# Kernel optimization log

Measured on AMD Instinct MI355X. Metric: run time of the kernel, lower is better.

Reference implementation:

```python
import jax, jax.numpy as jnp
import numpy as np

NH, KD, VD, C = 8, 64, 64, 256

def conv1x1(x, w, b):
    # x: (B,C,D,H,W), w: (O,C), b: (O,)
    return jnp.einsum('bcdhw,oc->bodhw', x, w) + b[None, :, None, None, None]

def setup_inputs() -> dict:
    key = jax.random.key(0)
    ks = jax.random.split(key, 8)
    B, D, H, W = 2, 32, 32, 32
    s = 0.02
    return {
        'x': jax.random.normal(ks[0], (B, C, D, H, W), jnp.float32),
        'q_w': jax.random.normal(ks[1], (NH * KD, C), jnp.float32) * s,
        'q_b': jnp.zeros((NH * KD,), jnp.float32),
        'kv_w': jax.random.normal(ks[2], (KD + VD, C), jnp.float32) * s,
        'kv_b': jnp.zeros((KD + VD,), jnp.float32),
        'proj_w': jax.random.normal(ks[3], (C, NH * VD), jnp.float32) * s,
        'proj_b': jnp.zeros((C,), jnp.float32),
        'layer_scale': jnp.full((C, 1, 1, 1), 1e-5, jnp.float32),
    }

def reference(x, q_w, q_b, kv_w, kv_b, proj_w, proj_b, layer_scale):
    B, Cc, D, H, W = x.shape
    scale = VD ** -0.5
    # q: (B, nh, D, H, W, kd) -> flatten(3,5) -> (B, nh, D, H*W*kd)
    q = conv1x1(x, q_w, q_b).reshape(B, NH, KD, D, H, W).transpose(0, 1, 3, 4, 5, 2)
    q = q.reshape(B, NH, D, H * W * KD)
    kv = conv1x1(x, kv_w, kv_b)  # (B, kd+vd, D, H, W)
    k = kv[:, :KD].transpose(0, 2, 3, 4, 1).reshape(B, D, H * W * KD)  # shared across heads
    v = kv[:, KD:].transpose(0, 2, 3, 4, 1).reshape(B, D, H * W * VD)
    attn = jax.nn.softmax(jnp.einsum('bnqf,bkf->bnqk', q, k) * scale, axis=-1)  # (B,nh,D,D)
    o = jnp.einsum('bnqk,bkf->bnqf', attn, v)  # (B, nh, D, H*W*vd)
    # transpose(1,2) then row-major reshape, exactly as torch
    o = o.transpose(0, 2, 1, 3).reshape(B, D, H, W, NH * VD).transpose(0, 4, 1, 2, 3)
    out = conv1x1(o, proj_w, proj_b)
    return out * layer_scale[None]
```

## Files before the change

kernel.cpp:

```cpp
#include <hip/hip_runtime.h>
#include <math.h>

#define SS 32768
#define FQL_LDS_BYTES 147456

typedef _Float16 half4v __attribute__((ext_vector_type(4)));
typedef _Float16 half8v __attribute__((ext_vector_type(8)));
typedef float float4v __attribute__((ext_vector_type(4)));

__device__ __forceinline__ void gload16(const void* g, void* l) {
    __builtin_amdgcn_global_load_lds(
        (const __attribute__((address_space(1))) unsigned int*)g,
        (__attribute__((address_space(3))) unsigned int*)l, 16, 0, 0);
}

__global__ __launch_bounds__(256)
void cvt_x_kernel(const float* __restrict__ x, _Float16* __restrict__ x_t)
{
    __shared__ float ls[64][65];
    const int b = blockIdx.z, c0 = blockIdx.y * 64, s0 = blockIdx.x * 64;
    const int t = threadIdx.x;
    const int tr = t >> 4, tc = t & 15;
#pragma unroll
    for (int p = 0; p < 4; p++) {
        int c_l = p * 16 + tr;
        float4v v = *(const float4v*)(x + (size_t)(b * 256 + c0 + c_l) * SS + s0 + tc * 4);
        ls[c_l][tc * 4 + 0] = v.x;
        ls[c_l][tc * 4 + 1] = v.y;
        ls[c_l][tc * 4 + 2] = v.z;
        ls[c_l][tc * 4 + 3] = v.w;
    }
    __syncthreads();
#pragma unroll
    for (int p = 0; p < 4; p++) {
        int s_l = p * 16 + tr;
        half4v h;
        h.x = (_Float16)ls[tc * 4 + 0][s_l];
        h.y = (_Float16)ls[tc * 4 + 1][s_l];
        h.z = (_Float16)ls[tc * 4 + 2][s_l];
        h.w = (_Float16)ls[tc * 4 + 3][s_l];
        *(half4v*)(x_t + ((size_t)b * SS + s0 + s_l) * 256 + c0 + tc * 4) = h;
    }
}

__global__ __launch_bounds__(256)
void cvt_w3_kernel(const float* __restrict__ s0, _Float16* __restrict__ d0,
                   const float* __restrict__ s1, _Float16* __restrict__ d1,
                   const float* __restrict__ s2, _Float16* __restrict__ d2)
{
    int bx = blockIdx.x;
    const float* s; _Float16* d; int base;
    if (bx < 128)      { s = s0; d = d0; base = bx; }
    else if (bx < 160) { s = s1; d = d1; base = bx - 128; }
    else               { s = s2; d = d2; base = bx - 160; }
    int i = (base * 256 + threadIdx.x) * 4;
    float4v v = *(const float4v*)(s + i);
    half4v h;
    h.x = (_Float16)v.x; h.y = (_Float16)v.y; h.z = (_Float16)v.z; h.w = (_Float16)v.w;
    *(half4v*)(d + i) = h;
}

__global__ __launch_bounds__(256)
void convkv_kernel(const _Float16* __restrict__ x_t,
                   const _Float16* __restrict__ wkv,
                   const float* __restrict__ kv_b,
                   _Float16* __restrict__ kv_t)
{
    __shared__ _Float16 smem[128 * 136];
    _Float16* const Ws = smem;
    _Float16* const Xs = smem + 128 * 64;
    const int b = blockIdx.y;
    const int s0 = blockIdx.x * 128;
    const int t = threadIdx.x;
    const int w = t >> 6, l = t & 63;
    const int om = (w & 1) * 64, sn = (w >> 1) * 64;

    const int lr = l >> 3;
    const int gch = ((l & 7) - lr) & 7;
    const int m15 = l & 15;
    const int sl0 = ((((l >> 4) + (l & 7)) & 7)) * 8;
    const int sl1 = ((((l >> 4) + 4 + (l & 7)) & 7)) * 8;

    float4v acc[4][4];
#pragma unroll
    for (int i = 0; i < 4; i++)
#pragma unroll
        for (int j = 0; j < 4; j++) acc[i][j] = (float4v){0.f, 0.f, 0.f, 0.f};

    const _Float16* wg = wkv + (size_t)(32 * w + lr) * 256 + gch * 8;
    const _Float16* xg = x_t + ((size_t)b * SS + s0 + 32 * w + lr) * 256 + gch * 8;
    _Float16* wl = &Ws[(32 * w) * 64];
    _Float16* xl = &Xs[(32 * w) * 64];

    for (int c0 = 0; c0 < 256; c0 += 64) {
#pragma unroll
        for (int rb = 0; rb < 4; rb++) {
            gload16(wg + (size_t)rb * 8 * 256 + c0, wl + rb * 8 * 64);
            gload16(xg + (size_t)rb * 8 * 256 + c0, xl + rb * 8 * 64);
        }
        __syncthreads();
#pragma unroll
        for (int ks = 0; ks < 2; ks++) {
            const int sl = ks ? sl1 : sl0;
            half8v a[4], bb[4];
#pragma unroll
            for (int i = 0; i < 4; i++)
                a[i] = *(const half8v*)&Ws[(om + i * 16 + m15) * 64 + sl];
#pragma unroll
            for (int j = 0; j < 4; j++)
                bb[j] = *(const half8v*)&Xs[(sn + j * 16 + m15) * 64 + sl];
#pragma unroll
            for (int i = 0; i < 4; i++)
#pragma unroll
                for (int j = 0; j < 4; j++)
                    acc[i][j] = __builtin_amdgcn_mfma_f32_16x16x32_f16(a[i], bb[j], acc[i][j], 0, 0, 0);
        }
        __syncthreads();
    }
    const int qd = l >> 4, m = l & 15;
#pragma unroll
    for (int i = 0; i < 4; i++) {
        float bv[4];
#pragma unroll
        for (int r = 0; r < 4; r++) bv[r] = kv_b[om + i * 16 + qd * 4 + r];
#pragma unroll
        for (int j = 0; j < 4; j++) {
            half4v h;
            h.x = (_Float16)(acc[i][j].x + bv[0]);
            h.y = (_Float16)(acc[i][j].y + bv[1]);
            h.z = (_Float16)(acc[i][j].z + bv[2]);
            h.w = (_Float16)(acc[i][j].w + bv[3]);
            int s_l = sn + j * 16 + m;
            *(half4v*)&smem[s_l * 136 + om + i * 16 + qd * 4] = h;
        }
    }
    __syncthreads();
    const int sr = t >> 4, kk = t & 15;
#pragma unroll
    for (int p = 0; p < 8; p++) {
        int s_l = p * 16 + sr;
        half8v h8 = *(const half8v*)&smem[s_l * 136 + kk * 8];
        *(half8v*)(kv_t + ((size_t)b * SS + s0 + s_l) * 128 + kk * 8) = h8;
    }
}

__global__ __launch_bounds__(512)
void fq_logits_kernel(const _Float16* __restrict__ x_t,
                      const _Float16* __restrict__ wq,
                      const float* __restrict__ q_b,
                      const _Float16* __restrict__ kv_t,
                      float* __restrict__ Lpart)
{
    extern __shared__ _Float16 sm[];
    _Float16* const Xs = sm;
    _Float16* const W0 = sm + 32768;
    _Float16* const W1 = sm + 49152;
    _Float16* const Qs = sm + 65536;

    const int chunk = blockIdx.x, b = blockIdx.y;
    const int hw0 = chunk * 4;
    const int t = threadIdx.x;
    const int w = t >> 6, l = t & 63;
    const int lq = l >> 4;
    const int l15 = l & 15;
    const int rh = l >> 5, ch = l & 31;

#pragma unroll
    for (int i = 0; i < 8; i++) {
        int r = w * 16 + i * 2 + rh;
        int qd = r >> 2, hwl = r & 3;
        int sc = ch ^ (r & 7);
        gload16(x_t + ((size_t)b * SS + qd * 1024 + hw0 + hwl) * 256 + sc * 8,
                Xs + (w * 16 + i * 2) * 256);
    }
#pragma unroll
    for (int i = 0; i < 4; i++) {
        int r = w * 8 + i * 2 + rh;
        int sc = ch ^ (r & 7);
        gload16(wq + (size_t)r * 256 + sc * 8, W0 + (w * 8 + i * 2) * 256);
    }

    half8v bk[8];
    if (w < 4) {
        const int nj = w & 1;
        const int kd = nj * 16 + l15;
        const _Float16* kbase = kv_t + ((size_t)b * SS + (size_t)kd * 1024 + hw0) * 128;
#pragma unroll
        for (int ks = 0; ks < 8; ks++) {
            int kk = ks * 32 + lq * 8;
            bk[ks] = *(const half8v*)(kbase + (size_t)(kk >> 6) * 128 + (kk & 63));
        }
    }
    __syncthreads();

    const int wm = w >> 2, wn = w & 3;
    const int m0 = wm * 32, n0 = wn * 32;
    float* const lp_base = Lpart + (((size_t)chunk * 2 + b) * 8) * 1024;

    for (int nh = 0; nh < 8; nh++) {
        _Float16* const Wcur = (nh & 1) ? W1 : W0;
        if (nh < 7) {
            _Float16* const Wnxt = (nh & 1) ? W0 : W1;
#pragma unroll
            for (int i = 0; i < 4; i++) {
                int r = w * 8 + i * 2 + rh;
                int sc = ch ^ (r & 7);
                gload16(wq + ((size_t)((nh + 1) * 64 + r)) * 256 + sc * 8,
                        Wnxt + (w * 8 + i * 2) * 256);
            }
        }
        float4v qacc[2][2];
#pragma unroll
        for (int i = 0; i < 2; i++)
#pragma unroll
            for (int j = 0; j < 2; j++) qacc[i][j] = (float4v){0.f, 0.f, 0.f, 0.f};
#pragma unroll
        for (int ks = 0; ks < 8; ks++) {
            int c8 = (ks * 32 + lq * 8) ^ ((l & 7) << 3);
            half8v a0 = *(const half8v*)&Wcur[(m0 + l15) * 256 + c8];
            half8v a1 = *(const half8v*)&Wcur[(m0 + 16 + l15) * 256 + c8];
            half8v x0 = *(const half8v*)&Xs[(n0 + l15) * 256 + c8];
            half8v x1 = *(const half8v*)&Xs[(n0 + 16 + l15) * 256 + c8];
            qacc[0][0] = __builtin_amdgcn_mfma_f32_16x16x32_f16(a0, x0, qacc[0][0], 0, 0, 0);
            qacc[0][1] = __builtin_amdgcn_mfma_f32_16x16x32_f16(a0, x1, qacc[0][1], 0, 0, 0);
            qacc[1][0] = __builtin_amdgcn_mfma_f32_16x16x32_f16(a1, x0, qacc[1][0], 0, 0, 0);
            qacc[1][1] = __builtin_amdgcn_mfma_f32_16x16x32_f16(a1, x1, qacc[1][1], 0, 0, 0);
        }
        __syncthreads();
#pragma unroll
        for (int i = 0; i < 2; i++) {
            int kbase = m0 + i * 16 + lq * 4;
            float4v bv = *(const float4v*)(q_b + nh * 64 + kbase);
#pragma unroll
            for (int j = 0; j < 2; j++) {
                int sp = n0 + j * 16 + l15;
                int key = ((sp ^ (sp >> 2)) & 7) << 3;
                half4v h;
                h.x = (_Float16)(qacc[i][j].x + bv.x);
                h.y = (_Float16)(qacc[i][j].y + bv.y);
                h.z = (_Float16)(qacc[i][j].z + bv.z);
                h.w = (_Float16)(qacc[i][j].w + bv.w);
                *(half4v*)&Qs[sp * 64 + (kbase ^ key)] = h;
            }
        }
        __syncthreads();
        if (w < 4) {
            const int mi = w >> 1, nj = w & 1;
            const int qd = mi * 16 + l15;
            float4v lacc = (float4v){0.f, 0.f, 0.f, 0.f};
#pragma unroll
            for (int ks = 0; ks < 8; ks++) {
                int kk = ks * 32 + lq * 8;
                int sp = qd * 4 + (kk >> 6);
                int key = ((sp ^ (sp >> 2)) & 7) << 3;
                half8v a = *(const half8v*)&Qs[sp * 64 + ((kk & 63) ^ key)];
                lacc = __builtin_amdgcn_mfma_f32_16x16x32_f16(a, bk[ks], lacc, 0, 0, 0);
            }
            float* dst = lp_base + (size_t)nh * 1024;
#pragma unroll
            for (int rr = 0; rr < 4; rr++)
                dst[(mi * 16 + lq * 4 + rr) * 32 + nj * 16 + l15] = lacc[rr];
        }
    }
}

__global__ __launch_bounds__(256)
void softmax_kernel(const float* __restrict__ Lpart, float* __restrict__ Lsm)
{
    __shared__ float red[32][8][32];
    const int t = threadIdx.x;
    const int rl = t & 7, cs = t >> 3;
    const int row = blockIdx.x * 8 + rl;
    const int b = row >> 8, nh = (row >> 5) & 7, qd = row & 31;
    float4v p[8];
#pragma unroll
    for (int j4 = 0; j4 < 8; j4++) p[j4] = (float4v){0.f, 0.f, 0.f, 0.f};
    for (int cc = 0; cc < 8; cc++) {
        int chunk = cs + cc * 32;
        const float* src = Lpart + (((size_t)chunk * 2 + b) * 8 + nh) * 1024 + qd * 32;
#pragma unroll
        for (int j4 = 0; j4 < 8; j4++) p[j4] += *(const float4v*)(src + j4 * 4);
    }
#pragma unroll
    for (int j4 = 0; j4 < 8; j4++) *(float4v*)&red[cs][rl][j4 * 4] = p[j4];
    __syncthreads();
    const int r2 = t >> 5, j = t & 31;
    float s = 0.f;
#pragma unroll
    for (int c2 = 0; c2 < 32; c2++) s += red[c2][r2][j];
    float mx = s;
#pragma unroll
    for (int off = 16; off >= 1; off >>= 1) mx = fmaxf(mx, __shfl_xor(mx, off, 32));
    float e = expf((s - mx) * 0.125f);
    float sum = e;
#pragma unroll
    for (int off = 16; off >= 1; off >>= 1) sum += __shfl_xor(sum, off, 32);
    Lsm[(size_t)(blockIdx.x * 8 + r2) * 32 + j] = e / sum;
}

__global__ __launch_bounds__(256)
void attn_v_kernel(const _Float16* __restrict__ kv_t,
                   const float* __restrict__ attn,
                   _Float16* __restrict__ o_t)
{
    __shared__ float as_[2048];
    const int wq = blockIdx.x, hl = blockIdx.y;
    const int b = blockIdx.z >> 2, rc = blockIdx.z & 3;
    const int t = threadIdx.x;
    {
        const float* src = attn + (size_t)b * 8192 + rc * 2048;
#pragma unroll
        for (int ll = 0; ll < 2; ll++) {
            int idx = (t + ll * 256) * 4;
            *(float4v*)(&as_[idx]) = *(const float4v*)(src + idx);
        }
    }
    __syncthreads();
    const int q4 = t & 127;
    const int half = t >> 7;
    const int tt = q4 >> 4;
    const int vd = (q4 * 4) & 63;
    const int hw = hl * 256 + wq * 8 + tt;
    float4v vreg[32];
#pragma unroll
    for (int j = 0; j < 32; j++) {
        half4v hv = *(const half4v*)(kv_t + ((size_t)((b * 32 + j) * 1024 + hw)) * 128 + 64 + vd);
        vreg[j] = (float4v){(float)hv.x, (float)hv.y, (float)hv.z, (float)hv.w};
    }
    _Float16* outb = o_t + (size_t)b * SS * 512;
#pragma unroll 2
    for (int rr = 0; rr < 32; rr++) {
        int row_l = half * 32 + rr;
        int row = rc * 64 + row_l;
        int hh = row >> 5, d = row & 31;
        const float* arow = &as_[row_l * 32];
        float ax = 0.f, ay = 0.f, az = 0.f, aw = 0.f;
#pragma unroll
        for (int j4 = 0; j4 < 8; j4++) {
            float4v a4 = *(const float4v*)(&arow[j4 * 4]);
            float4v v0 = vreg[j4 * 4 + 0];
            float4v v1 = vreg[j4 * 4 + 1];
            float4v v2 = vreg[j4 * 4 + 2];
            float4v v3 = vreg[j4 * 4 + 3];
            ax = fmaf(a4.x, v0.x, ax); ay = fmaf(a4.x, v0.y, ay);
            az = fmaf(a4.x, v0.z, az); aw = fmaf(a4.x, v0.w, aw);
            ax = fmaf(a4.y, v1.x, ax); ay = fmaf(a4.y, v1.y, ay);
            az = fmaf(a4.y, v1.z, az); aw = fmaf(a4.y, v1.w, aw);
            ax = fmaf(a4.z, v2.x, ax); ay = fmaf(a4.z, v2.y, ay);
            az = fmaf(a4.z, v2.z, az); aw = fmaf(a4.z, v2.w, aw);
            ax = fmaf(a4.w, v3.x, ax); ay = fmaf(a4.w, v3.y, ay);
            az = fmaf(a4.w, v3.z, az); aw = fmaf(a4.w, v3.w, aw);
        }
        int hp = hh * 4 + hl;
        size_t sp = (size_t)d * 1024 + hp * 32 + wq;
        half4v o4;
        o4.x = (_Float16)ax; o4.y = (_Float16)ay; o4.z = (_Float16)az; o4.w = (_Float16)aw;
        *(half4v*)(outb + sp * 512 + q4 * 4) = o4;
    }
}

__global__ __launch_bounds__(256)
void proj_mfma_kernel(const _Float16* __restrict__ o_t,
                      const _Float16* __restrict__ wp,
                      const float* __restrict__ pb,
                      const float* __restrict__ ls,
                      float* __restrict__ out)
{
    __shared__ _Float16 Ws[128 * 64];
    __shared__ _Float16 Xs[128 * 64];
    const int b = blockIdx.y;
    const int bx = blockIdx.x;
    const int grp = bx >> 4, rem = bx & 15;
    const int s_tile = grp * 8 + (rem & 7);
    const int o_tile = rem >> 3;
    const int s0 = s_tile * 128, o0 = o_tile * 128;
    const int t = threadIdx.x;
    const int w = t >> 6, l = t & 63;
    const int om = (w & 1) * 64, sn = (w >> 1) * 64;

    const int lr = l >> 3;
    const int gch = ((l & 7) - lr) & 7;
    const int m15 = l & 15;
    const int sl0 = ((((l >> 4) + (l & 7)) & 7)) * 8;
    const int sl1 = ((((l >> 4) + 4 + (l & 7)) & 7)) * 8;

    float4v acc[4][4];
#pragma unroll
    for (int i = 0; i < 4; i++)
#pragma unroll
        for (int j = 0; j < 4; j++) acc[i][j] = (float4v){0.f, 0.f, 0.f, 0.f};

    const _Float16* wg = wp + (size_t)(o0 + 32 * w + lr) * 512 + gch * 8;
    const _Float16* xg = o_t + ((size_t)b * SS + s0 + 32 * w + lr) * 512 + gch * 8;
    _Float16* wl = &Ws[(32 * w) * 64];
    _Float16* xl = &Xs[(32 * w) * 64];

    for (int c0 = 0; c0 < 512; c0 += 64) {
#pragma unroll
        for (int rb = 0; rb < 4; rb++) {
            gload16(wg + (size_t)rb * 8 * 512 + c0, wl + rb * 8 * 64);
            gload16(xg + (size_t)rb * 8 * 512 + c0, xl + rb * 8 * 64);
        }
        __syncthreads();
#pragma unroll
        for (int ks = 0; ks < 2; ks++) {
            const int sl = ks ? sl1 : sl0;
            half8v a[4], bb[4];
#pragma unroll
            for (int i = 0; i < 4; i++)
                a[i] = *(const half8v*)&Ws[(om + i * 16 + m15) * 64 + sl];
#pragma unroll
            for (int j = 0; j < 4; j++)
                bb[j] = *(const half8v*)&Xs[(sn + j * 16 + m15) * 64 + sl];
#pragma unroll
            for (int i = 0; i < 4; i++)
#pragma unroll
                for (int j = 0; j < 4; j++)
                    acc[i][j] = __builtin_amdgcn_mfma_f32_16x16x32_f16(a[i], bb[j], acc[i][j], 0, 0, 0);
        }
        __syncthreads();
    }
    const int qd = l >> 4, m = l & 15;
#pragma unroll
    for (int i = 0; i < 4; i++) {
        float pbv[4], lsv[4];
#pragma unroll
        for (int r = 0; r < 4; r++) {
            int o = o0 + om + i * 16 + qd * 4 + r;
            pbv[r] = pb[o];
            lsv[r] = ls[o];
        }
#pragma unroll
        for (int j = 0; j < 4; j++) {
            int s = s0 + sn + j * 16 + m;
#pragma unroll
            for (int r = 0; r < 4; r++) {
                int o = o0 + om + i * 16 + qd * 4 + r;
                out[((size_t)b * 256 + o) * SS + s] = (acc[i][j][r] + pbv[r]) * lsv[r];
            }
        }
    }
}

extern "C" void kernel_launch(void* const* d_in, const int* in_sizes, int n_in,
                              void* d_out, int out_size, void* d_ws, size_t ws_size,
                              hipStream_t stream)
{
    const float* x      = (const float*)d_in[0];
    const float* q_w    = (const float*)d_in[1];
    const float* q_b    = (const float*)d_in[2];
    const float* kv_w   = (const float*)d_in[3];
    const float* kv_b   = (const float*)d_in[4];
    const float* proj_w = (const float*)d_in[5];
    const float* proj_b = (const float*)d_in[6];
    const float* ls     = (const float*)d_in[7];
    float* out = (float*)d_out;

    char* ws = (char*)d_ws;
    _Float16* x_t  = (_Float16*)(ws);
    _Float16* o_t  = (_Float16*)(ws + 33554432);
    float*    Lpart= (float*)   (ws + 33554432);
    _Float16* kv_t = (_Float16*)(ws + 100663296);
    float*    Lsm  = (float*)   (ws + 117440512);
    _Float16* wq   = (_Float16*)(ws + 117506048);
    _Float16* wkv  = (_Float16*)(ws + 117768192);
    _Float16* wp   = (_Float16*)(ws + 117833728);

    static bool fql_attr_set = false;
    if (!fql_attr_set) {
        hipFuncSetAttribute(reinterpret_cast<const void*>(fq_logits_kernel),
                            hipFuncAttributeMaxDynamicSharedMemorySize, FQL_LDS_BYTES);
        fql_attr_set = true;
    }

    cvt_x_kernel<<<dim3(512, 4, 2), 256, 0, stream>>>(x, x_t);
    cvt_w3_kernel<<<dim3(288), 256, 0, stream>>>(q_w, wq, kv_w, wkv, proj_w, wp);

    convkv_kernel<<<dim3(256, 2), 256, 0, stream>>>(x_t, wkv, kv_b, kv_t);
    fq_logits_kernel<<<dim3(256, 2), 512, FQL_LDS_BYTES, stream>>>(x_t, wq, q_b, kv_t, Lpart);
    softmax_kernel<<<dim3(64), 256, 0, stream>>>(Lpart, Lsm);
    attn_v_kernel<<<dim3(32, 4, 8), 256, 0, stream>>>(kv_t, Lsm, o_t);
    proj_mfma_kernel<<<dim3(512, 2), 256, 0, stream>>>(o_t, wp, proj_b, ls, out);
}
```

Measured before the change: 259.2 us.

## Restructure Q-logits kernel: fragment-major weights in registers, per-head wave pairs

```diff
diff --git a/kernel.cpp b/kernel.cpp
--- a/kernel.cpp
+++ b/kernel.cpp
@@ -2,7 +2,7 @@
 #include <math.h>
 
 #define SS 32768
-#define FQL_LDS_BYTES 147456
+#define FQL_LDS_BYTES 149504
 
 typedef _Float16 half4v __attribute__((ext_vector_type(4)));
 typedef _Float16 half8v __attribute__((ext_vector_type(8)));
@@ -49,15 +49,28 @@
                    const float* __restrict__ s2, _Float16* __restrict__ d2)
 {
     int bx = blockIdx.x;
-    const float* s; _Float16* d; int base;
-    if (bx < 128)      { s = s0; d = d0; base = bx; }
-    else if (bx < 160) { s = s1; d = d1; base = bx - 128; }
-    else               { s = s2; d = d2; base = bx - 160; }
-    int i = (base * 256 + threadIdx.x) * 4;
-    float4v v = *(const float4v*)(s + i);
-    half4v h;
-    h.x = (_Float16)v.x; h.y = (_Float16)v.y; h.z = (_Float16)v.z; h.w = (_Float16)v.w;
-    *(half4v*)(d + i) = h;
+    if (bx < 128) {
+        int idx = (bx * 256 + threadIdx.x) * 4;
+        int e = idx & 7;
+        int lane = (idx >> 3) & 63;
+        int l15 = lane & 15, lq = lane >> 4;
+        int blk = idx >> 9;
+        int i = blk & 3, ks = (blk >> 2) & 7, nh = blk >> 5;
+        const float* src = s0 + (size_t)(nh * 64 + i * 16 + l15) * 256 + ks * 32 + lq * 8 + e;
+        float4v v = *(const float4v*)src;
+        half4v hh;
+        hh.x = (_Float16)v.x; hh.y = (_Float16)v.y; hh.z = (_Float16)v.z; hh.w = (_Float16)v.w;
+        *(half4v*)(d0 + idx) = hh;
+    } else {
+        const float* s; _Float16* d; int base;
+        if (bx < 160) { s = s1; d = d1; base = bx - 128; }
+        else          { s = s2; d = d2; base = bx - 160; }
+        int i = (base * 256 + threadIdx.x) * 4;
+        float4v v = *(const float4v*)(s + i);
+        half4v hh;
+        hh.x = (_Float16)v.x; hh.y = (_Float16)v.y; hh.z = (_Float16)v.z; hh.w = (_Float16)v.w;
+        *(half4v*)(d + i) = hh;
+    }
 }
 
 __global__ __launch_bounds__(256)
@@ -146,120 +159,144 @@
 
 __global__ __launch_bounds__(512)
 void fq_logits_kernel(const _Float16* __restrict__ x_t,
-                      const _Float16* __restrict__ wq,
+                      const _Float16* __restrict__ wq_f,
                       const float* __restrict__ q_b,
                       const _Float16* __restrict__ kv_t,
                       float* __restrict__ Lpart)
 {
     extern __shared__ _Float16 sm[];
     _Float16* const Xs = sm;
-    _Float16* const W0 = sm + 32768;
-    _Float16* const W1 = sm + 49152;
-    _Float16* const Qs = sm + 65536;
+    _Float16* const Qs = sm + 32768;
+    float* const scr = (float*)(sm + 65536);
 
     const int chunk = blockIdx.x, b = blockIdx.y;
     const int hw0 = chunk * 4;
     const int t = threadIdx.x;
     const int w = t >> 6, l = t & 63;
-    const int lq = l >> 4;
-    const int l15 = l & 15;
-    const int rh = l >> 5, ch = l & 31;
-
-#pragma unroll
-    for (int i = 0; i < 8; i++) {
-        int r = w * 16 + i * 2 + rh;
+    const int l15 = l & 15, lq = l >> 4;
+    const int h = w >> 1;
+    const int ns = w & 1;
+    const int n0 = ns * 64;
+
+#pragma unroll
+    for (int ii = 0; ii < 8; ii++) {
+        int r = w * 16 + ii * 2 + (l >> 5);
+        int p = l & 31;
+        int sc = (p - 4 * r) & 31;
         int qd = r >> 2, hwl = r & 3;
-        int sc = ch ^ (r & 7);
         gload16(x_t + ((size_t)b * SS + qd * 1024 + hw0 + hwl) * 256 + sc * 8,
-                Xs + (w * 16 + i * 2) * 256);
-    }
-#pragma unroll
-    for (int i = 0; i < 4; i++) {
-        int r = w * 8 + i * 2 + rh;
-        int sc = ch ^ (r & 7);
-        gload16(wq + (size_t)r * 256 + sc * 8, W0 + (w * 8 + i * 2) * 256);
+                Xs + (w * 16 + ii * 2) * 256);
     }
 
     half8v bk[8];
-    if (w < 4) {
-        const int nj = w & 1;
-        const int kd = nj * 16 + l15;
-        const _Float16* kbase = kv_t + ((size_t)b * SS + (size_t)kd * 1024 + hw0) * 128;
+#pragma unroll
+    for (int j = 0; j < 2; j++)
+#pragma unroll
+        for (int ksp = 0; ksp < 4; ksp++) {
+            int kk = (ns * 4 + ksp) * 32 + lq * 8;
+            bk[j * 4 + ksp] = *(const half8v*)(kv_t +
+                ((size_t)b * SS + (size_t)(j * 16 + l15) * 1024 + hw0 + (kk >> 6)) * 128 + (kk & 63));
+        }
+    __syncthreads();
+
+    _Float16* const Qs_h = Qs + h * 8192;
+    float* const scr_h = scr + h * (32 * 36);
+    float* const lp_g = Lpart + (((size_t)chunk * 2 + b) * 8) * 1024;
+
+    for (int g = 0; g < 2; g++) {
+        const int nh = g * 4 + h;
+        const _Float16* wf = wq_f + ((size_t)nh * 32) * 512 + (size_t)l * 8;
+        half8v aF[4], aN[4];
+#pragma unroll
+        for (int i = 0; i < 4; i++) aF[i] = *(const half8v*)(wf + (size_t)i * 512);
+        float4v acc[4][4];
+#pragma unroll
+        for (int i = 0; i < 4; i++)
+#pragma unroll
+            for (int j = 0; j < 4; j++) acc[i][j] = (float4v){0.f, 0.f, 0.f, 0.f};
 #pragma unroll
         for (int ks = 0; ks < 8; ks++) {
-            int kk = ks * 32 + lq * 8;
-            bk[ks] = *(const half8v*)(kbase + (size_t)(kk >> 6) * 128 + (kk & 63));
-        }
-    }
-    __syncthreads();
-
-    const int wm = w >> 2, wn = w & 3;
-    const int m0 = wm * 32, n0 = wn * 32;
-    float* const lp_base = Lpart + (((size_t)chunk * 2 + b) * 8) * 1024;
-
-    for (int nh = 0; nh < 8; nh++) {
-        _Float16* const Wcur = (nh & 1) ? W1 : W0;
-        if (nh < 7) {
-            _Float16* const Wnxt = (nh & 1) ? W0 : W1;
-#pragma unroll
-            for (int i = 0; i < 4; i++) {
-                int r = w * 8 + i * 2 + rh;
-                int sc = ch ^ (r & 7);
-                gload16(wq + ((size_t)((nh + 1) * 64 + r)) * 256 + sc * 8,
-                        Wnxt + (w * 8 + i * 2) * 256);
+            if (ks < 7) {
+#pragma unroll
+                for (int i = 0; i < 4; i++)
+                    aN[i] = *(const half8v*)(wf + (size_t)((ks + 1) * 4 + i) * 512);
             }
-        }
-        float4v qacc[2][2];
-#pragma unroll
-        for (int i = 0; i < 2; i++)
-#pragma unroll
-            for (int j = 0; j < 2; j++) qacc[i][j] = (float4v){0.f, 0.f, 0.f, 0.f};
-#pragma unroll
-        for (int ks = 0; ks < 8; ks++) {
-            int c8 = (ks * 32 + lq * 8) ^ ((l & 7) << 3);
-            half8v a0 = *(const half8v*)&Wcur[(m0 + l15) * 256 + c8];
-            half8v a1 = *(const half8v*)&Wcur[(m0 + 16 + l15) * 256 + c8];
-            half8v x0 = *(const half8v*)&Xs[(n0 + l15) * 256 + c8];
-            half8v x1 = *(const half8v*)&Xs[(n0 + 16 + l15) * 256 + c8];
-            qacc[0][0] = __builtin_amdgcn_mfma_f32_16x16x32_f16(a0, x0, qacc[0][0], 0, 0, 0);
-            qacc[0][1] = __builtin_amdgcn_mfma_f32_16x16x32_f16(a0, x1, qacc[0][1], 0, 0, 0);
-            qacc[1][0] = __builtin_amdgcn_mfma_f32_16x16x32_f16(a1, x0, qacc[1][0], 0, 0, 0);
-            qacc[1][1] = __builtin_amdgcn_mfma_f32_16x16x32_f16(a1, x1, qacc[1][1], 0, 0, 0);
-        }
-        __syncthreads();
-#pragma unroll
-        for (int i = 0; i < 2; i++) {
-            int kbase = m0 + i * 16 + lq * 4;
-            float4v bv = *(const float4v*)(q_b + nh * 64 + kbase);
-#pragma unroll
-            for (int j = 0; j < 2; j++) {
+            const int p8 = (((ks * 4 + lq) + 4 * (l15 & 7)) & 31) * 8;
+            half8v bF[4];
+#pragma unroll
+            for (int j = 0; j < 4; j++)
+                bF[j] = *(const half8v*)&Xs[(n0 + j * 16 + l15) * 256 + p8];
+#pragma unroll
+            for (int i = 0; i < 4; i++)
+#pragma unroll
+                for (int j = 0; j < 4; j++)
+                    acc[i][j] = __builtin_amdgcn_mfma_f32_16x16x32_f16(aF[i], bF[j], acc[i][j], 0, 0, 0);
+#pragma unroll
+            for (int i = 0; i < 4; i++) aF[i] = aN[i];
+        }
+#pragma unroll
+        for (int i = 0; i < 4; i++) {
+            int kb = i * 16 + lq * 4;
+            float4v bv = *(const float4v*)(q_b + nh * 64 + kb);
+#pragma unroll
+            for (int j = 0; j < 4; j++) {
                 int sp = n0 + j * 16 + l15;
                 int key = ((sp ^ (sp >> 2)) & 7) << 3;
-                half4v h;
-                h.x = (_Float16)(qacc[i][j].x + bv.x);
-                h.y = (_Float16)(qacc[i][j].y + bv.y);
-                h.z = (_Float16)(qacc[i][j].z + bv.z);
-                h.w = (_Float16)(qacc[i][j].w + bv.w);
-                *(half4v*)&Qs[sp * 64 + (kbase ^ key)] = h;
+                half4v hv;
+                hv.x = (_Float16)(acc[i][j].x + bv.x);
+                hv.y = (_Float16)(acc[i][j].y + bv.y);
+                hv.z = (_Float16)(acc[i][j].z + bv.z);
+                hv.w = (_Float16)(acc[i][j].w + bv.w);
+                *(half4v*)&Qs_h[sp * 64 + (kb ^ key)] = hv;
             }
         }
         __syncthreads();
-        if (w < 4) {
-            const int mi = w >> 1, nj = w & 1;
-            const int qd = mi * 16 + l15;
-            float4v lacc = (float4v){0.f, 0.f, 0.f, 0.f};
-#pragma unroll
-            for (int ks = 0; ks < 8; ks++) {
-                int kk = ks * 32 + lq * 8;
-                int sp = qd * 4 + (kk >> 6);
+        float4v lacc[2][2];
+#pragma unroll
+        for (int i = 0; i < 2; i++)
+#pragma unroll
+            for (int j = 0; j < 2; j++) lacc[i][j] = (float4v){0.f, 0.f, 0.f, 0.f};
+#pragma unroll
+        for (int ksp = 0; ksp < 4; ksp++) {
+            int kk = (ns * 4 + ksp) * 32 + lq * 8;
+            half8v a0, a1;
+            {
+                int sp = l15 * 4 + (kk >> 6);
                 int key = ((sp ^ (sp >> 2)) & 7) << 3;
-                half8v a = *(const half8v*)&Qs[sp * 64 + ((kk & 63) ^ key)];
-                lacc = __builtin_amdgcn_mfma_f32_16x16x32_f16(a, bk[ks], lacc, 0, 0, 0);
+                a0 = *(const half8v*)&Qs_h[sp * 64 + ((kk & 63) ^ key)];
             }
-            float* dst = lp_base + (size_t)nh * 1024;
-#pragma unroll
-            for (int rr = 0; rr < 4; rr++)
-                dst[(mi * 16 + lq * 4 + rr) * 32 + nj * 16 + l15] = lacc[rr];
+            {
+                int sp = (16 + l15) * 4 + (kk >> 6);
+                int key = ((sp ^ (sp >> 2)) & 7) << 3;
+                a1 = *(const half8v*)&Qs_h[sp * 64 + ((kk & 63) ^ key)];
+            }
+            lacc[0][0] = __builtin_amdgcn_mfma_f32_16x16x32_f16(a0, bk[ksp],     lacc[0][0], 0, 0, 0);
+            lacc[0][1] = __builtin_amdgcn_mfma_f32_16x16x32_f16(a0, bk[4 + ksp], lacc[0][1], 0, 0, 0);
+            lacc[1][0] = __builtin_amdgcn_mfma_f32_16x16x32_f16(a1, bk[ksp],     lacc[1][0], 0, 0, 0);
+            lacc[1][1] = __builtin_amdgcn_mfma_f32_16x16x32_f16(a1, bk[4 + ksp], lacc[1][1], 0, 0, 0);
+        }
+        if (ns == 1) {
+#pragma unroll
+            for (int i = 0; i < 2; i++)
+#pragma unroll
+                for (int j = 0; j < 2; j++)
+                    *(float4v*)&scr_h[(j * 16 + l15) * 36 + i * 16 + lq * 4] = lacc[i][j];
+        }
+        __syncthreads();
+        if (ns == 0) {
+            float* dst = lp_g + (size_t)nh * 1024;
+#pragma unroll
+            for (int i = 0; i < 2; i++)
+#pragma unroll
+                for (int j = 0; j < 2; j++) {
+                    float4v o = lacc[i][j];
+                    float4v p4 = *(const float4v*)&scr_h[(j * 16 + l15) * 36 + i * 16 + lq * 4];
+                    o += p4;
+                    int rb = i * 16 + lq * 4;
+#pragma unroll
+                    for (int rr = 0; rr < 4; rr++)
+                        dst[(rb + rr) * 32 + j * 16 + l15] = o[rr];
+                }
         }
     }
 }
@@ -462,7 +499,7 @@
     float*    Lpart= (float*)   (ws + 33554432);
     _Float16* kv_t = (_Float16*)(ws + 100663296);
     float*    Lsm  = (float*)   (ws + 117440512);
-    _Float16* wq   = (_Float16*)(ws + 117506048);
+    _Float16* wq_f = (_Float16*)(ws + 117506048);
     _Float16* wkv  = (_Float16*)(ws + 117768192);
     _Float16* wp   = (_Float16*)(ws + 117833728);
 
@@ -474,10 +511,10 @@
     }
 
     cvt_x_kernel<<<dim3(512, 4, 2), 256, 0, stream>>>(x, x_t);
-    cvt_w3_kernel<<<dim3(288), 256, 0, stream>>>(q_w, wq, kv_w, wkv, proj_w, wp);
+    cvt_w3_kernel<<<dim3(288), 256, 0, stream>>>(q_w, wq_f, kv_w, wkv, proj_w, wp);
 
     convkv_kernel<<<dim3(256, 2), 256, 0, stream>>>(x_t, wkv, kv_b, kv_t);
-    fq_logits_kernel<<<dim3(256, 2), 512, FQL_LDS_BYTES, stream>>>(x_t, wq, q_b, kv_t, Lpart);
+    fq_logits_kernel<<<dim3(256, 2), 512, FQL_LDS_BYTES, stream>>>(x_t, wq_f, q_b, kv_t, Lpart);
     softmax_kernel<<<dim3(64), 256, 0, stream>>>(Lpart, Lsm);
     attn_v_kernel<<<dim3(32, 4, 8), 256, 0, stream>>>(kv_t, Lsm, o_t);
     proj_mfma_kernel<<<dim3(512, 2), 256, 0, stream>>>(o_t, wp, proj_b, ls, out);
```

Result: faster. 242.1 us (-6.6%).
